# Kernel tuning notes

Hardware: AMD Instinct MI355X
Metric: run time of the kernel (lower is better)

The kernel has to match this reference:

```python
import jax, jax.numpy as jnp
import numpy as np

B, S, D, H = 2, 2048, 1024, 16
HW = D // H  # head width = 64


def setup_inputs() -> dict:
    key = jax.random.key(0)
    ks = jax.random.split(key, 9)
    x = jax.random.normal(ks[0], (B, S, D), dtype=jnp.float32)
    mask = jax.random.randint(ks[1], (B, S), 0, 2, dtype=jnp.int32)
    pos = jax.random.normal(ks[2], (B, S, S), dtype=jnp.float32) * 0.02
    wq = jax.random.normal(ks[3], (D, D), dtype=jnp.float32) * 0.02
    bq = jnp.zeros((D,), dtype=jnp.float32)
    wk = jax.random.normal(ks[4], (D, D), dtype=jnp.float32) * 0.02
    bk = jnp.zeros((D,), dtype=jnp.float32)
    wv = jax.random.normal(ks[5], (D, D), dtype=jnp.float32) * 0.02
    bv = jnp.zeros((D,), dtype=jnp.float32)
    return {"x": x, "mask": mask, "pos": pos,
            "wq": wq, "bq": bq, "wk": wk, "bk": bk, "wv": wv, "bv": bv}


def reference(x, mask, pos, wq, bq, wk, bk, wv, bv):
    # QKV projections (torch Linear: y = x @ W^T + b)
    q = (x @ wq.T + bq).reshape(B, S, H, HW)
    k = (x @ wk.T + bk).reshape(B, S, H, HW)
    v = (x @ wv.T + bv).reshape(B, S, H, HW)
    # scores: (B, H, Sq, Sk)
    scores = jnp.einsum('bqhd,bkhd->bhqk', q, k) / jnp.sqrt(jnp.float32(HW))
    scores = scores + pos[:, None, :, :]
    m = mask.astype(jnp.float32)[:, None, None, :]
    scores = scores - 10000.0 * (1.0 - m)
    attn = jax.nn.softmax(scores, axis=-1)  # dropout p=0 (inference)
    h = jnp.einsum('bhqk,bkhd->bqhd', attn, v).reshape(B, S, D)
    return h
```

## Files before the change

kernel.cpp:

```cpp
#include <hip/hip_runtime.h>

#define B_ 2
#define S_ 2048
#define D_ 1024
#define H_ 16
#define HW_ 64
#define NT_ (S_ / 64)

typedef __attribute__((ext_vector_type(8))) short s16x8;
typedef __attribute__((ext_vector_type(4))) float f32x4;
typedef __attribute__((ext_vector_type(2))) unsigned int u32x2;
typedef __attribute__((ext_vector_type(4))) unsigned int u32x4;

__device__ __forceinline__ unsigned short f2bf(float f) {
  unsigned int x = __builtin_bit_cast(unsigned int, f);
  x += 0x7fffu + ((x >> 16) & 1u);
  return (unsigned short)(x >> 16);
}
__device__ __forceinline__ unsigned int cvtpk_bf16(float lo, float hi) {
  unsigned int r;
  asm("v_cvt_pk_bf16_f32 %0, %1, %2" : "=v"(r) : "v"(lo), "v"(hi));
  return r;
}
__device__ __forceinline__ void gload16(const void* g, void* l) {
  __builtin_amdgcn_global_load_lds(
      (const __attribute__((address_space(1))) unsigned int*)g,
      (__attribute__((address_space(3))) unsigned int*)l, 16, 0, 0);
}

__global__ __launch_bounds__(256) void cvt_all(const float* __restrict__ x,
                                               const float* __restrict__ wq,
                                               const float* __restrict__ wk,
                                               const float* __restrict__ wv,
                                               const float* __restrict__ pos,
                                               const int* __restrict__ mask,
                                               unsigned short* __restrict__ xb,
                                               unsigned short* __restrict__ wb,
                                               unsigned short* __restrict__ posb) {
  const int blk = blockIdx.x;
  if (blk < 2048) {
    int i = blk * 256 + threadIdx.x;
    const float4* s = (const float4*)x;
    float4 a = s[2 * i], b = s[2 * i + 1];
    s16x8 o;
    o[0] = (short)f2bf(a.x); o[1] = (short)f2bf(a.y);
    o[2] = (short)f2bf(a.z); o[3] = (short)f2bf(a.w);
    o[4] = (short)f2bf(b.x); o[5] = (short)f2bf(b.y);
    o[6] = (short)f2bf(b.z); o[7] = (short)f2bf(b.w);
    ((s16x8*)xb)[i] = o;
  } else if (blk < 3584) {
    int blk2 = blk - 2048;
    const float* src = (blk2 < 512) ? wq : (blk2 < 1024) ? wk : wv;
    int i = (blk2 & 511) * 256 + threadIdx.x;
    const float4* s = (const float4*)src;
    float4 a = s[2 * i], b = s[2 * i + 1];
    s16x8 o;
    o[0] = (short)f2bf(a.x); o[1] = (short)f2bf(a.y);
    o[2] = (short)f2bf(a.z); o[3] = (short)f2bf(a.w);
    o[4] = (short)f2bf(b.x); o[5] = (short)f2bf(b.y);
    o[6] = (short)f2bf(b.z); o[7] = (short)f2bf(b.w);
    ((s16x8*)wb)[(size_t)(blk2 >> 9) * (D_ * D_ / 8) + i] = o;
  } else {
    int i = (blk - 3584) * 256 + threadIdx.x;
    int e = i * 8;
    int b = e / (S_ * S_);
    int k = e & (S_ - 1);
    const float4* s = (const float4*)pos;
    float4 a = s[2 * i], c = s[2 * i + 1];
    const int* mrow = mask + b * S_ + k;
    const float L2E = 1.4426950408889634f;
    float f[8] = {a.x, a.y, a.z, a.w, c.x, c.y, c.z, c.w};
    s16x8 o;
#pragma unroll
    for (int j = 0; j < 8; ++j) {
      float bias = mrow[j] ? 0.0f : -14427.0f;
      o[j] = (short)f2bf(f[j] * L2E + bias);
    }
    ((s16x8*)posb)[i] = o;
  }
}

__global__ __launch_bounds__(256) void qkv_gemm(const unsigned short* __restrict__ X,
                                                const unsigned short* __restrict__ W3,
                                                const float* __restrict__ bq,
                                                const float* __restrict__ bk,
                                                const float* __restrict__ bv,
                                                unsigned short* __restrict__ O3,
                                                unsigned short* __restrict__ VT) {
  const int mat = blockIdx.z;
  const unsigned short* Wp = W3 + (size_t)mat * (D_ * D_);
  const float* bias = (mat == 0) ? bq : (mat == 1) ? bk : bv;
  unsigned short* Op = O3 + (size_t)mat * ((size_t)B_ * S_ * D_);

  const int bm = blockIdx.y * 128, bn = blockIdx.x * 128;
  const int tid = threadIdx.x;
  const int lane = tid & 63, w = tid >> 6;
  const int wr = (w >> 1) * 64, wc = (w & 1) * 64;
  const int l15 = lane & 15, lh = lane >> 4;

  __shared__ __align__(16) unsigned short Al[128 * 64];
  __shared__ __align__(16) unsigned short Wl[128 * 64];

  f32x4 acc[4][4];
#pragma unroll
  for (int m = 0; m < 4; ++m)
#pragma unroll
    for (int n = 0; n < 4; ++n) acc[m][n] = (f32x4){0.f, 0.f, 0.f, 0.f};

  const int srow = lane >> 3;
  const int scol = ((lane & 7) ^ srow) * 8;
  const int i0 = w * 4;

  for (int k0 = 0; k0 < D_; k0 += 64) {
    __syncthreads();
#pragma unroll
    for (int i2 = 0; i2 < 4; ++i2) {
      int i = i0 + i2;
      int row = 8 * i + srow;
      gload16(X + (size_t)(bm + row) * D_ + k0 + scol, Al + i * 512);
      gload16(Wp + (size_t)(bn + row) * D_ + k0 + scol, Wl + i * 512);
    }
    __syncthreads();
#pragma unroll
    for (int kb = 0; kb < 2; ++kb) {
      const int cs = (kb * 32 + lh * 8) ^ ((l15 & 7) * 8);
      s16x8 af[4], wf[4];
#pragma unroll
      for (int m = 0; m < 4; ++m)
        af[m] = *(const s16x8*)(Al + (wr + m * 16 + l15) * 64 + cs);
#pragma unroll
      for (int n = 0; n < 4; ++n)
        wf[n] = *(const s16x8*)(Wl + (wc + n * 16 + l15) * 64 + cs);
      if (mat == 2) {
#pragma unroll
        for (int m = 0; m < 4; ++m)
#pragma unroll
          for (int n = 0; n < 4; ++n)
            acc[m][n] =
                __builtin_amdgcn_mfma_f32_16x16x32_bf16(wf[n], af[m], acc[m][n], 0, 0, 0);
      } else {
#pragma unroll
        for (int m = 0; m < 4; ++m)
#pragma unroll
          for (int n = 0; n < 4; ++n)
            acc[m][n] =
                __builtin_amdgcn_mfma_f32_16x16x32_bf16(af[m], wf[n], acc[m][n], 0, 0, 0);
      }
    }
  }

  if (mat == 2) {
#pragma unroll
    for (int n = 0; n < 4; ++n) {
      f32x4 b4 = *(const f32x4*)(bias + bn + wc + n * 16 + lh * 4);
#pragma unroll
      for (int m = 0; m < 4; ++m) {
        int t = bm + wr + m * 16 + l15;
        int bb = t >> 11, s = t & (S_ - 1);
#pragma unroll
        for (int r = 0; r < 4; ++r) {
          int f = bn + wc + n * 16 + lh * 4 + r;
          VT[((size_t)(bb * H_ + (f >> 6)) * HW_ + (f & 63)) * S_ + s] =
              f2bf(acc[m][n][r] + b4[r]);
        }
      }
    }
  } else {
    const float oscale = (mat == 0) ? 0.18033688751411092f : 1.0f;
#pragma unroll
    for (int n = 0; n < 4; ++n) {
      int col = bn + wc + n * 16 + l15;
      float bval = bias[col];
#pragma unroll
      for (int m = 0; m < 4; ++m) {
        int row0 = bm + wr + m * 16 + lh * 4;
#pragma unroll
        for (int r = 0; r < 4; ++r)
          Op[(size_t)(row0 + r) * D_ + col] = f2bf((acc[m][n][r] + bval) * oscale);
      }
    }
  }
}

__global__ __launch_bounds__(256, 4) void attn_kernel(
    const unsigned short* __restrict__ Q,
    const unsigned short* __restrict__ K,
    const unsigned short* __restrict__ VT,
    const unsigned short* __restrict__ POSM,
    float* __restrict__ OUT) {
  const int h = blockIdx.x, qt = blockIdx.y, b = blockIdx.z;
  const int tid = threadIdx.x;
  const int lane = tid & 63, w = tid >> 6;
  const int l15 = lane & 15, lh = lane >> 4;

  __shared__ __align__(16) unsigned short Kl[2][64 * 64];
  __shared__ __align__(16) unsigned short Vl[2][64 * 64];

  const int swzk = ((l15 & 3) | (((l15 >> 2) & 1) << 2)) * 8;
  const int swzv = ((l15 & 3) | ((l15 & 8) >> 1)) * 8;
  const int rowbase = 8 * (l15 >> 2) + (l15 & 3);

  const int srow = lane >> 3;
  const int scol = ((lane & 7) ^ ((lane >> 3) & 3) ^ ((w & 1) << 2)) * 8;
  const unsigned short* Kbase = K + (size_t)b * S_ * D_ + h * HW_;
  const unsigned short* Vbase = VT + ((size_t)(b * H_ + h) * HW_) * S_;

  auto stage = [&](int buf, int kt) {
    const int k0 = kt * 64;
#pragma unroll
    for (int i = 0; i < 2; ++i) {
      const int rb = i * 32 + w * 8;
      gload16(Kbase + (size_t)(k0 + rb + srow) * D_ + scol, &Kl[buf][rb * 64]);
      gload16(Vbase + (size_t)(rb + srow) * S_ + k0 + scol, &Vl[buf][rb * 64]);
    }
  };

  const int q0 = qt * 64 + w * 16;
  const int qg = q0 + l15;
  const unsigned short* Pp = POSM + (size_t)(b * S_ + qg) * S_ + lh * 8;

  u32x2 pmw_c[4], pmw_n[4];
#pragma unroll
  for (int n = 0; n < 4; ++n)
    pmw_c[n] = *(const u32x2*)(Pp + (n >> 1) * 32 + (n & 1) * 4);
  stage(0, 0);

  s16x8 qf[2];
  {
    const unsigned short* qp = Q + (size_t)(b * S_ + qg) * D_ + h * HW_ + lh * 8;
    qf[0] = *(const s16x8*)qp;
    qf[1] = *(const s16x8*)(qp + 32);
  }

  f32x4 Oc[4];
#pragma unroll
  for (int n = 0; n < 4; ++n) Oc[n] = (f32x4){0.f, 0.f, 0.f, 0.f};
  f32x4 lsum = (f32x4){0.f, 0.f, 0.f, 0.f};

  for (int kt = 0; kt < NT_; ++kt) {
    const int cur = kt & 1;

    if (kt + 1 < NT_) {
#pragma unroll
      for (int n = 0; n < 4; ++n)
        pmw_n[n] = *(const u32x2*)(Pp + (kt + 1) * 64 + (n >> 1) * 32 + (n & 1) * 4);
      stage(cur ^ 1, kt + 1);
      asm volatile("s_waitcnt vmcnt(8)" ::: "memory");
    } else {
      asm volatile("s_waitcnt vmcnt(0)" ::: "memory");
    }
    asm volatile("s_barrier" ::: "memory");

    const unsigned short* Kc = Kl[cur];
    const unsigned short* Vc = Vl[cur];

    f32x4 sc[4];
    __builtin_amdgcn_s_setprio(1);
#pragma unroll
    for (int n = 0; n < 4; ++n) {
      const unsigned short* kr = Kc + (rowbase + (n & 1) * 4 + (n >> 1) * 32) * 64;
      s16x8 kf0 = *(const s16x8*)(kr + ((lh * 8) ^ swzk));
      s16x8 kf1 = *(const s16x8*)(kr + ((32 + lh * 8) ^ swzk));
      f32x4 c;
      c[0] = __builtin_bit_cast(float, pmw_c[n][0] << 16);
      c[1] = __builtin_bit_cast(float, pmw_c[n][0] & 0xffff0000u);
      c[2] = __builtin_bit_cast(float, pmw_c[n][1] << 16);
      c[3] = __builtin_bit_cast(float, pmw_c[n][1] & 0xffff0000u);
      c = __builtin_amdgcn_mfma_f32_16x16x32_bf16(kf0, qf[0], c, 0, 0, 0);
      c = __builtin_amdgcn_mfma_f32_16x16x32_bf16(kf1, qf[1], c, 0, 0, 0);
      sc[n] = c;
    }
    __builtin_amdgcn_s_setprio(0);

#pragma unroll
    for (int n = 0; n < 4; ++n)
#pragma unroll
      for (int r = 0; r < 4; ++r) {
        float p = __builtin_amdgcn_exp2f(sc[n][r]);
        sc[n][r] = p;
        lsum[n] += p;
      }

    __builtin_amdgcn_s_setprio(1);
#pragma unroll
    for (int kb = 0; kb < 2; ++kb) {
      u32x4 pw;
      pw[0] = cvtpk_bf16(sc[2 * kb][0], sc[2 * kb][1]);
      pw[1] = cvtpk_bf16(sc[2 * kb][2], sc[2 * kb][3]);
      pw[2] = cvtpk_bf16(sc[2 * kb + 1][0], sc[2 * kb + 1][1]);
      pw[3] = cvtpk_bf16(sc[2 * kb + 1][2], sc[2 * kb + 1][3]);
      s16x8 pf = __builtin_bit_cast(s16x8, pw);
#pragma unroll
      for (int n = 0; n < 4; ++n) {
        s16x8 vf = *(const s16x8*)(Vc + (n * 16 + l15) * 64 + ((kb * 32 + lh * 8) ^ swzv));
        Oc[n] = __builtin_amdgcn_mfma_f32_16x16x32_bf16(vf, pf, Oc[n], 0, 0, 0);
      }
    }
    __builtin_amdgcn_s_setprio(0);

    asm volatile("s_barrier" ::: "memory");

#pragma unroll
    for (int n = 0; n < 4; ++n) pmw_c[n] = pmw_n[n];
  }

  float lrow = (lsum[0] + lsum[1]) + (lsum[2] + lsum[3]);
  lrow += __shfl_xor(lrow, 16, 64);
  lrow += __shfl_xor(lrow, 32, 64);
  float inv = 1.0f / lrow;
  float* outp = OUT + (size_t)(b * S_ + qg) * D_ + h * HW_ + lh * 4;
#pragma unroll
  for (int n = 0; n < 4; ++n) {
    f32x4 o;
#pragma unroll
    for (int r = 0; r < 4; ++r) o[r] = Oc[n][r] * inv;
    *(f32x4*)(outp + n * 16) = o;
  }
}

extern "C" void kernel_launch(void* const* d_in, const int* in_sizes, int n_in,
                              void* d_out, int out_size, void* d_ws, size_t ws_size,
                              hipStream_t stream) {
  const float* x   = (const float*)d_in[0];
  const int*   msk = (const int*)d_in[1];
  const float* pos = (const float*)d_in[2];
  const float* wq  = (const float*)d_in[3];
  const float* bq  = (const float*)d_in[4];
  const float* wk  = (const float*)d_in[5];
  const float* bk  = (const float*)d_in[6];
  const float* wv  = (const float*)d_in[7];
  const float* bv  = (const float*)d_in[8];
  float* out = (float*)d_out;

  char* ws = (char*)d_ws;
  unsigned short* xb   = (unsigned short*)(ws);
  unsigned short* wb   = (unsigned short*)(ws + 8388608);
  unsigned short* qkv  = (unsigned short*)(ws + 14680064);
  unsigned short* posb = (unsigned short*)(ws + 39845888);
  unsigned short* vt   = (unsigned short*)(ws + 56623104);

  cvt_all<<<7680, 256, 0, stream>>>(x, wq, wk, wv, pos, msk, xb, wb, posb);

  qkv_gemm<<<dim3(D_ / 128, (B_ * S_) / 128, 3), 256, 0, stream>>>(
      xb, wb, bq, bk, bv, qkv, vt);

  attn_kernel<<<dim3(H_, S_ / 64, B_), 256, 0, stream>>>(
      qkv, qkv + (size_t)B_ * S_ * D_, vt, posb, out);
}
```

Before: 121.5 us.

## Split attention key range in two and merge partial results in a combine kernel

Splits the key dimension of the attention kernel into two halves. Each half runs as its own block, giving twice as many blocks. Each block writes its unnormalized output and row sum: one half goes to a workspace buffer, the other straight to the output. A new combine kernel adds the two partials and divides by the summed row sums. This is meant to raise parallelism and shorten each block's serial loop, at the cost of extra global memory traffic and one more launch. The workspace layout is also repacked.

Result: slower. 130.1 us (+7.1%).

```diff
diff --git a/kernel.cpp b/kernel.cpp
--- a/kernel.cpp
+++ b/kernel.cpp
@@ -6,6 +6,8 @@
 #define H_ 16
 #define HW_ 64
 #define NT_ (S_ / 64)
+#define NSPLIT_ 2
+#define TPS_ (NT_ / NSPLIT_)
 
 typedef __attribute__((ext_vector_type(8))) short s16x8;
 typedef __attribute__((ext_vector_type(4))) float f32x4;
@@ -187,8 +189,11 @@
     const unsigned short* __restrict__ K,
     const unsigned short* __restrict__ VT,
     const unsigned short* __restrict__ POSM,
+    float* __restrict__ OP0,
+    float* __restrict__ LP,
     float* __restrict__ OUT) {
-  const int h = blockIdx.x, qt = blockIdx.y, b = blockIdx.z;
+  const int h = blockIdx.x, qt = blockIdx.y;
+  const int b = blockIdx.z & (B_ - 1), sp = blockIdx.z >> 1;
   const int tid = threadIdx.x;
   const int lane = tid & 63, w = tid >> 6;
   const int l15 = lane & 15, lh = lane >> 4;
@@ -215,6 +220,7 @@
     }
   };
 
+  const int kt0 = sp * TPS_;
   const int q0 = qt * 64 + w * 16;
   const int qg = q0 + l15;
   const unsigned short* Pp = POSM + (size_t)(b * S_ + qg) * S_ + lh * 8;
@@ -222,8 +228,8 @@
   u32x2 pmw_c[4], pmw_n[4];
 #pragma unroll
   for (int n = 0; n < 4; ++n)
-    pmw_c[n] = *(const u32x2*)(Pp + (n >> 1) * 32 + (n & 1) * 4);
-  stage(0, 0);
+    pmw_c[n] = *(const u32x2*)(Pp + kt0 * 64 + (n >> 1) * 32 + (n & 1) * 4);
+  stage(0, kt0);
 
   s16x8 qf[2];
   {
@@ -237,10 +243,11 @@
   for (int n = 0; n < 4; ++n) Oc[n] = (f32x4){0.f, 0.f, 0.f, 0.f};
   f32x4 lsum = (f32x4){0.f, 0.f, 0.f, 0.f};
 
-  for (int kt = 0; kt < NT_; ++kt) {
-    const int cur = kt & 1;
-
-    if (kt + 1 < NT_) {
+  for (int t = 0; t < TPS_; ++t) {
+    const int kt = kt0 + t;
+    const int cur = t & 1;
+
+    if (t + 1 < TPS_) {
 #pragma unroll
       for (int n = 0; n < 4; ++n)
         pmw_n[n] = *(const u32x2*)(Pp + (kt + 1) * 64 + (n >> 1) * 32 + (n & 1) * 4);
@@ -307,15 +314,33 @@
   float lrow = (lsum[0] + lsum[1]) + (lsum[2] + lsum[3]);
   lrow += __shfl_xor(lrow, 16, 64);
   lrow += __shfl_xor(lrow, 32, 64);
-  float inv = 1.0f / lrow;
-  float* outp = OUT + (size_t)(b * S_ + qg) * D_ + h * HW_ + lh * 4;
-#pragma unroll
-  for (int n = 0; n < 4; ++n) {
-    f32x4 o;
-#pragma unroll
-    for (int r = 0; r < 4; ++r) o[r] = Oc[n][r] * inv;
-    *(f32x4*)(outp + n * 16) = o;
-  }
+  if (lh == 0)
+    LP[(size_t)sp * (B_ * H_ * S_) + ((size_t)b * H_ + h) * S_ + qg] = lrow;
+
+  float* outp = (sp ? OUT : OP0) + (size_t)(b * S_ + qg) * D_ + h * HW_ + lh * 4;
+#pragma unroll
+  for (int n = 0; n < 4; ++n)
+    *(f32x4*)(outp + n * 16) = Oc[n];
+}
+
+__global__ __launch_bounds__(256) void combine_kernel(const float* __restrict__ OP0,
+                                                      const float* __restrict__ LP,
+                                                      float* __restrict__ OUT) {
+  int i = blockIdx.x * 256 + threadIdx.x;
+  int e = i * 8;
+  int bb = e >> 21;
+  int s = (e >> 10) & (S_ - 1);
+  int h = (e & (D_ - 1)) >> 6;
+  size_t li = ((size_t)bb * H_ + h) * S_ + s;
+  float l0 = LP[li];
+  float l1 = LP[(size_t)(B_ * H_ * S_) + li];
+  float inv = 1.0f / (l0 + l1);
+  f32x4 a0 = *(const f32x4*)(OP0 + e), a1 = *(const f32x4*)(OP0 + e + 4);
+  f32x4 b0 = *(const f32x4*)(OUT + e), b1 = *(const f32x4*)(OUT + e + 4);
+#pragma unroll
+  for (int r = 0; r < 4; ++r) { b0[r] = (a0[r] + b0[r]) * inv; b1[r] = (a1[r] + b1[r]) * inv; }
+  *(f32x4*)(OUT + e) = b0;
+  *(f32x4*)(OUT + e + 4) = b1;
 }
 
 extern "C" void kernel_launch(void* const* d_in, const int* in_sizes, int n_in,
@@ -336,14 +361,18 @@
   unsigned short* xb   = (unsigned short*)(ws);
   unsigned short* wb   = (unsigned short*)(ws + 8388608);
   unsigned short* qkv  = (unsigned short*)(ws + 14680064);
-  unsigned short* posb = (unsigned short*)(ws + 39845888);
-  unsigned short* vt   = (unsigned short*)(ws + 56623104);
+  unsigned short* posb = (unsigned short*)(ws + 31457280);
+  unsigned short* vt   = (unsigned short*)(ws + 48234496);
+  float*          op0  = (float*)(ws + 56623104);
+  float*          lp   = (float*)(ws + 73400320);
 
   cvt_all<<<7680, 256, 0, stream>>>(x, wq, wk, wv, pos, msk, xb, wb, posb);
 
   qkv_gemm<<<dim3(D_ / 128, (B_ * S_) / 128, 3), 256, 0, stream>>>(
       xb, wb, bq, bk, bv, qkv, vt);
 
-  attn_kernel<<<dim3(H_, S_ / 64, B_), 256, 0, stream>>>(
-      qkv, qkv + (size_t)B_ * S_ * D_, vt, posb, out);
-}
+  attn_kernel<<<dim3(H_, S_ / 64, B_ * NSPLIT_), 256, 0, stream>>>(
+      qkv, qkv + (size_t)B_ * S_ * D_, vt, posb, op0, lp, out);
+
+  combine_kernel<<<(B_ * S_ * D_) / (256 * 8), 256, 0, stream>>>(op0, lp, out);
+}
```

## Split attention waves over query pairs and key halves with LDS reduction

Applied to the files above, without the earlier changes.

Each attention wave now computes 32 query rows against one 32-key half of each key tile, rather than 16 query rows against the full 64 keys. K fragments are reused across two query subtiles, and V fragments are loaded once per tile. The two key-half partial outputs and row sums are combined through shared memory at the end. Position bias is fetched as one 16-byte vector per row instead of four 8-byte loads, and the workspace offsets are compacted. The trade-off is more accumulator registers and an extra epilogue reduction with two block barriers.

Measured after the change: 118.6 us. 1.02x faster.

```diff
diff --git a/kernel.cpp b/kernel.cpp
--- a/kernel.cpp
+++ b/kernel.cpp
@@ -16,6 +16,10 @@
   unsigned int x = __builtin_bit_cast(unsigned int, f);
   x += 0x7fffu + ((x >> 16) & 1u);
   return (unsigned short)(x >> 16);
+}
+__device__ __forceinline__ float bf2f(unsigned short u) {
+  unsigned int x = ((unsigned int)u) << 16;
+  return __builtin_bit_cast(float, x);
 }
 __device__ __forceinline__ unsigned int cvtpk_bf16(float lo, float hi) {
   unsigned int r;
@@ -192,13 +196,14 @@
   const int tid = threadIdx.x;
   const int lane = tid & 63, w = tid >> 6;
   const int l15 = lane & 15, lh = lane >> 4;
+  const int qp = w >> 1, kh = w & 1;
 
   __shared__ __align__(16) unsigned short Kl[2][64 * 64];
   __shared__ __align__(16) unsigned short Vl[2][64 * 64];
 
   const int swzk = ((l15 & 3) | (((l15 >> 2) & 1) << 2)) * 8;
   const int swzv = ((l15 & 3) | ((l15 & 8) >> 1)) * 8;
-  const int rowbase = 8 * (l15 >> 2) + (l15 & 3);
+  const int rowbase = kh * 32 + 8 * (l15 >> 2) + (l15 & 3);
 
   const int srow = lane >> 3;
   const int scol = ((lane & 7) ^ ((lane >> 3) & 3) ^ ((w & 1) << 2)) * 8;
@@ -215,37 +220,41 @@
     }
   };
 
-  const int q0 = qt * 64 + w * 16;
-  const int qg = q0 + l15;
-  const unsigned short* Pp = POSM + (size_t)(b * S_ + qg) * S_ + lh * 8;
-
-  u32x2 pmw_c[4], pmw_n[4];
-#pragma unroll
-  for (int n = 0; n < 4; ++n)
-    pmw_c[n] = *(const u32x2*)(Pp + (n >> 1) * 32 + (n & 1) * 4);
+  const int q0 = qt * 64 + qp * 32;
+  const int qg0 = q0 + l15, qg1 = q0 + 16 + l15;
+  const unsigned short* Pp0 = POSM + (size_t)(b * S_ + qg0) * S_ + kh * 32 + lh * 8;
+  const unsigned short* Pp1 = POSM + (size_t)(b * S_ + qg1) * S_ + kh * 32 + lh * 8;
+
+  s16x8 pm_c[2], pm_n[2];
+  pm_c[0] = *(const s16x8*)(Pp0);
+  pm_c[1] = *(const s16x8*)(Pp1);
   stage(0, 0);
 
-  s16x8 qf[2];
+  s16x8 qf[2][2];
   {
-    const unsigned short* qp = Q + (size_t)(b * S_ + qg) * D_ + h * HW_ + lh * 8;
-    qf[0] = *(const s16x8*)qp;
-    qf[1] = *(const s16x8*)(qp + 32);
-  }
-
-  f32x4 Oc[4];
-#pragma unroll
-  for (int n = 0; n < 4; ++n) Oc[n] = (f32x4){0.f, 0.f, 0.f, 0.f};
-  f32x4 lsum = (f32x4){0.f, 0.f, 0.f, 0.f};
+    const unsigned short* qp0 = Q + (size_t)(b * S_ + qg0) * D_ + h * HW_ + lh * 8;
+    const unsigned short* qp1 = Q + (size_t)(b * S_ + qg1) * D_ + h * HW_ + lh * 8;
+    qf[0][0] = *(const s16x8*)qp0;
+    qf[0][1] = *(const s16x8*)(qp0 + 32);
+    qf[1][0] = *(const s16x8*)qp1;
+    qf[1][1] = *(const s16x8*)(qp1 + 32);
+  }
+
+  f32x4 Oc[2][4];
+#pragma unroll
+  for (int s = 0; s < 2; ++s)
+#pragma unroll
+    for (int n = 0; n < 4; ++n) Oc[s][n] = (f32x4){0.f, 0.f, 0.f, 0.f};
+  float lsq[2] = {0.f, 0.f};
 
   for (int kt = 0; kt < NT_; ++kt) {
     const int cur = kt & 1;
 
     if (kt + 1 < NT_) {
-#pragma unroll
-      for (int n = 0; n < 4; ++n)
-        pmw_n[n] = *(const u32x2*)(Pp + (kt + 1) * 64 + (n >> 1) * 32 + (n & 1) * 4);
+      pm_n[0] = *(const s16x8*)(Pp0 + (kt + 1) * 64);
+      pm_n[1] = *(const s16x8*)(Pp1 + (kt + 1) * 64);
       stage(cur ^ 1, kt + 1);
-      asm volatile("s_waitcnt vmcnt(8)" ::: "memory");
+      asm volatile("s_waitcnt vmcnt(6)" ::: "memory");
     } else {
       asm volatile("s_waitcnt vmcnt(0)" ::: "memory");
     }
@@ -254,67 +263,100 @@
     const unsigned short* Kc = Kl[cur];
     const unsigned short* Vc = Vl[cur];
 
-    f32x4 sc[4];
+    s16x8 kf0[2], kf1[2];
+#pragma unroll
+    for (int n = 0; n < 2; ++n) {
+      const unsigned short* kr = Kc + (rowbase + n * 4) * 64;
+      kf0[n] = *(const s16x8*)(kr + ((lh * 8) ^ swzk));
+      kf1[n] = *(const s16x8*)(kr + ((32 + lh * 8) ^ swzk));
+    }
+
+    f32x4 sc[2][2];
     __builtin_amdgcn_s_setprio(1);
 #pragma unroll
-    for (int n = 0; n < 4; ++n) {
-      const unsigned short* kr = Kc + (rowbase + (n & 1) * 4 + (n >> 1) * 32) * 64;
-      s16x8 kf0 = *(const s16x8*)(kr + ((lh * 8) ^ swzk));
-      s16x8 kf1 = *(const s16x8*)(kr + ((32 + lh * 8) ^ swzk));
-      f32x4 c;
-      c[0] = __builtin_bit_cast(float, pmw_c[n][0] << 16);
-      c[1] = __builtin_bit_cast(float, pmw_c[n][0] & 0xffff0000u);
-      c[2] = __builtin_bit_cast(float, pmw_c[n][1] << 16);
-      c[3] = __builtin_bit_cast(float, pmw_c[n][1] & 0xffff0000u);
-      c = __builtin_amdgcn_mfma_f32_16x16x32_bf16(kf0, qf[0], c, 0, 0, 0);
-      c = __builtin_amdgcn_mfma_f32_16x16x32_bf16(kf1, qf[1], c, 0, 0, 0);
-      sc[n] = c;
-    }
+    for (int s = 0; s < 2; ++s)
+#pragma unroll
+      for (int n = 0; n < 2; ++n) {
+        f32x4 c;
+#pragma unroll
+        for (int r = 0; r < 4; ++r)
+          c[r] = bf2f((unsigned short)pm_c[s][n * 4 + r]);
+        c = __builtin_amdgcn_mfma_f32_16x16x32_bf16(kf0[n], qf[s][0], c, 0, 0, 0);
+        c = __builtin_amdgcn_mfma_f32_16x16x32_bf16(kf1[n], qf[s][1], c, 0, 0, 0);
+        sc[s][n] = c;
+      }
     __builtin_amdgcn_s_setprio(0);
 
 #pragma unroll
+    for (int s = 0; s < 2; ++s)
+#pragma unroll
+      for (int n = 0; n < 2; ++n)
+#pragma unroll
+        for (int r = 0; r < 4; ++r) {
+          float p = __builtin_amdgcn_exp2f(sc[s][n][r]);
+          sc[s][n][r] = p;
+          lsq[s] += p;
+        }
+
+    __builtin_amdgcn_s_setprio(1);
+    s16x8 vf[4];
+#pragma unroll
     for (int n = 0; n < 4; ++n)
-#pragma unroll
-      for (int r = 0; r < 4; ++r) {
-        float p = __builtin_amdgcn_exp2f(sc[n][r]);
-        sc[n][r] = p;
-        lsum[n] += p;
-      }
-
-    __builtin_amdgcn_s_setprio(1);
-#pragma unroll
-    for (int kb = 0; kb < 2; ++kb) {
+      vf[n] = *(const s16x8*)(Vc + (n * 16 + l15) * 64 + ((kh * 32 + lh * 8) ^ swzv));
+#pragma unroll
+    for (int s = 0; s < 2; ++s) {
       u32x4 pw;
-      pw[0] = cvtpk_bf16(sc[2 * kb][0], sc[2 * kb][1]);
-      pw[1] = cvtpk_bf16(sc[2 * kb][2], sc[2 * kb][3]);
-      pw[2] = cvtpk_bf16(sc[2 * kb + 1][0], sc[2 * kb + 1][1]);
-      pw[3] = cvtpk_bf16(sc[2 * kb + 1][2], sc[2 * kb + 1][3]);
+      pw[0] = cvtpk_bf16(sc[s][0][0], sc[s][0][1]);
+      pw[1] = cvtpk_bf16(sc[s][0][2], sc[s][0][3]);
+      pw[2] = cvtpk_bf16(sc[s][1][0], sc[s][1][1]);
+      pw[3] = cvtpk_bf16(sc[s][1][2], sc[s][1][3]);
       s16x8 pf = __builtin_bit_cast(s16x8, pw);
 #pragma unroll
+      for (int n = 0; n < 4; ++n)
+        Oc[s][n] = __builtin_amdgcn_mfma_f32_16x16x32_bf16(vf[n], pf, Oc[s][n], 0, 0, 0);
+    }
+    __builtin_amdgcn_s_setprio(0);
+
+    asm volatile("s_barrier" ::: "memory");
+
+    pm_c[0] = pm_n[0];
+    pm_c[1] = pm_n[1];
+  }
+
+#pragma unroll
+  for (int s = 0; s < 2; ++s) {
+    lsq[s] += __shfl_xor(lsq[s], 16, 64);
+    lsq[s] += __shfl_xor(lsq[s], 32, 64);
+  }
+
+  __syncthreads();
+  f32x4* xO = (f32x4*)Kl;
+  float* xL = (float*)Vl;
+  if (kh) {
+#pragma unroll
+    for (int s = 0; s < 2; ++s) {
+#pragma unroll
+      for (int n = 0; n < 4; ++n)
+        xO[((qp * 2 + s) * 4 + n) * 64 + lane] = Oc[s][n];
+      if (lh == 0) xL[(qp * 2 + s) * 16 + l15] = lsq[s];
+    }
+  }
+  __syncthreads();
+  if (!kh) {
+#pragma unroll
+    for (int s = 0; s < 2; ++s) {
+      float ltot = lsq[s] + xL[(qp * 2 + s) * 16 + l15];
+      float inv = 1.0f / ltot;
+      int qg = q0 + s * 16 + l15;
+      float* outp = OUT + (size_t)(b * S_ + qg) * D_ + h * HW_ + lh * 4;
+#pragma unroll
       for (int n = 0; n < 4; ++n) {
-        s16x8 vf = *(const s16x8*)(Vc + (n * 16 + l15) * 64 + ((kb * 32 + lh * 8) ^ swzv));
-        Oc[n] = __builtin_amdgcn_mfma_f32_16x16x32_bf16(vf, pf, Oc[n], 0, 0, 0);
-      }
-    }
-    __builtin_amdgcn_s_setprio(0);
-
-    asm volatile("s_barrier" ::: "memory");
-
-#pragma unroll
-    for (int n = 0; n < 4; ++n) pmw_c[n] = pmw_n[n];
-  }
-
-  float lrow = (lsum[0] + lsum[1]) + (lsum[2] + lsum[3]);
-  lrow += __shfl_xor(lrow, 16, 64);
-  lrow += __shfl_xor(lrow, 32, 64);
-  float inv = 1.0f / lrow;
-  float* outp = OUT + (size_t)(b * S_ + qg) * D_ + h * HW_ + lh * 4;
-#pragma unroll
-  for (int n = 0; n < 4; ++n) {
-    f32x4 o;
-#pragma unroll
-    for (int r = 0; r < 4; ++r) o[r] = Oc[n][r] * inv;
-    *(f32x4*)(outp + n * 16) = o;
+        f32x4 o = xO[((qp * 2 + s) * 4 + n) * 64 + lane];
+#pragma unroll
+        for (int r = 0; r < 4; ++r) o[r] = (o[r] + Oc[s][n][r]) * inv;
+        *(f32x4*)(outp + n * 16) = o;
+      }
+    }
   }
 }
 
@@ -336,8 +378,8 @@
   unsigned short* xb   = (unsigned short*)(ws);
   unsigned short* wb   = (unsigned short*)(ws + 8388608);
   unsigned short* qkv  = (unsigned short*)(ws + 14680064);
-  unsigned short* posb = (unsigned short*)(ws + 39845888);
-  unsigned short* vt   = (unsigned short*)(ws + 56623104);
+  unsigned short* posb = (unsigned short*)(ws + 31457280);
+  unsigned short* vt   = (unsigned short*)(ws + 48234496);
 
   cvt_all<<<7680, 256, 0, stream>>>(x, wq, wk, wv, pos, msk, xb, wb, posb);
 
```
